# Kernel optimization log

Measured on AMD Instinct MI355X. Metric: run time of the kernel, lower is better.

The kernel has to match this reference:

```python
import jax, jax.numpy as jnp
import numpy as np

EPS_RMS = 1e-6
EPS_L2 = 1e-12  # torch F.normalize default eps


def _l2_normalize(x):
    n = jnp.sqrt(jnp.sum(x * x, axis=-1, keepdims=True))
    return x / jnp.maximum(n, EPS_L2)


def _dwconv(x, w, b):
    # depthwise Conv1d: x [B,L,D], w [D,1,K], b [D]; padding=K//2 (same length for odd K)
    K = w.shape[-1]
    y = jax.lax.conv_general_dilated(
        jnp.swapaxes(x, 1, 2), w, window_strides=(1,),
        padding=[(K // 2, K // 2)], feature_group_count=w.shape[0],
        dimension_numbers=('NCH', 'OIH', 'NCH'))
    return jnp.swapaxes(y + b[None, :, None], 1, 2)


def setup_inputs() -> dict:
    key = jax.random.key(0)
    ks = jax.random.split(key, 12)
    B, L, D, K = 8, 2048, 128, 3
    inp = {
        'x': jax.random.normal(ks[0], (B, L, D), dtype=jnp.float32),
        'state': jnp.zeros((B, D, D), dtype=jnp.float32),
        'W_in': jax.random.normal(ks[1], (4 * D, D), dtype=jnp.float32) * 0.02,
        'W_gate': jax.random.normal(ks[2], (2 * D, D), dtype=jnp.float32) * 0.02,
        'W_out': jax.random.normal(ks[3], (D, D), dtype=jnp.float32) * 0.02,
        'W_res': jax.random.normal(ks[4], (D, D), dtype=jnp.float32) * 0.02,
        'qconv_w': jax.random.normal(ks[5], (D, 1, K), dtype=jnp.float32) * 0.5,
        'qconv_b': jnp.zeros((D,), dtype=jnp.float32),
        'kconv_w': jax.random.normal(ks[6], (D, 1, K), dtype=jnp.float32) * 0.5,
        'kconv_b': jnp.zeros((D,), dtype=jnp.float32),
        'rms_w': jnp.ones((D,), dtype=jnp.float32),
    }
    return inp


def reference(x, state, W_in, W_gate, W_out, W_res,
              qconv_w, qconv_b, kconv_w, kconv_b, rms_w):
    B, L, D = x.shape
    residual = x @ W_res.T
    qkv = x @ W_in.T  # [B,L,4D]
    q, k, v, gate = jnp.split(qkv, 4, axis=-1)
    q = _l2_normalize(jax.nn.sigmoid(_dwconv(q, qconv_w, qconv_b)))
    k = _l2_normalize(jax.nn.sigmoid(_dwconv(k, kconv_w, kconv_b)))
    g = jax.nn.sigmoid(gate @ W_gate.T)  # [B,L,2D]
    alpha, beta = jnp.split(g, 2, axis=-1)

    # Delta-rule recurrence over time. State S [B,D,D] indexed S[b, v_dim, k_dim]:
    # S <- alpha_j * (S_ij - (S k)_i * beta_j k_j) + beta_j * v_i k_j ; out = silu(q @ S)
    def step(S, inp):
        q_t, k_t, v_t, a_t, b_t = inp  # each [B,D]
        Sk = jnp.einsum('bij,bj->bi', S, k_t)          # S @ k
        bk = b_t * k_t                                  # beta*k, column scaling
        S = a_t[:, None, :] * (S - Sk[:, :, None] * bk[:, None, :]) \
            + v_t[:, :, None] * bk[:, None, :]
        out_t = jax.nn.silu(jnp.einsum('bi,bij->bj', q_t, S))
        return S, out_t

    xs = tuple(jnp.swapaxes(a, 0, 1) for a in (q, k, v, alpha, beta))  # [L,B,D]
    S_fin, outs = jax.lax.scan(step, state, xs)
    out = jnp.swapaxes(outs, 0, 1) @ W_out.T  # [B,L,D]
    # dropout (p=0.125) is identity in eval mode
    out = out * jax.lax.rsqrt(jnp.mean(out * out, axis=-1, keepdims=True) + EPS_RMS) * rms_w
    out = out + residual
    return out, S_fin
```

## Files before the change

kernel.cpp:

```cpp
#include <hip/hip_runtime.h>
#include <hip/hip_bf16.h>
#include <math.h>

#define BB 8
#define LL 2048
#define LQ 512
#define DD 128

template <int CTRL>
__device__ __forceinline__ float dpp_add(float x) {
    int xi = __float_as_int(x);
    int yi = __builtin_amdgcn_update_dpp(xi, xi, CTRL, 0xF, 0xF, false);
    return x + __int_as_float(yi);
}
__device__ __forceinline__ float allreduce16(float p) {
    p = dpp_add<0xB1>(p);
    p = dpp_add<0x4E>(p);
    p = dpp_add<0x141>(p);
    p = dpp_add<0x140>(p);
    return p;
}
__device__ __forceinline__ float rlane(float p, int l) {
    return __int_as_float(__builtin_amdgcn_readlane(__float_as_int(p), l));
}

__global__ __launch_bounds__(256) void gemm_kernel(
    const float* __restrict__ X, long ldx, long sB, long sQ,
    const float* __restrict__ W,
    float* __restrict__ C, int ldc,
    int applySig)
{
    __shared__ float Xs[32 * 132];
    __shared__ float Ws[64 * 132];
    const int tid = threadIdx.x;
    const int m0 = blockIdx.x * 32;
    const int o0 = blockIdx.y * 64;
    {
        int row = tid >> 3, cg = tid & 7;
        int m = m0 + row;
        int b = m >> 11, t = m & 2047, qq = t >> 9, tl = t & 511;
        const float* src = X + (size_t)b * sB + (size_t)qq * sQ
                             + (size_t)tl * ldx + cg * 16;
        float* dst = Xs + row * 132 + cg * 16;
#pragma unroll
        for (int u = 0; u < 4; ++u)
            *(float4*)(dst + 4 * u) = *(const float4*)(src + 4 * u);
    }
    {
        int o = tid >> 2, cg = tid & 3;
        const float* src = W + (size_t)(o0 + o) * 128 + cg * 32;
        float* dst = Ws + o * 132 + cg * 32;
#pragma unroll
        for (int u = 0; u < 8; ++u)
            *(float4*)(dst + 4 * u) = *(const float4*)(src + 4 * u);
    }
    __syncthreads();
    const int tx = tid & 31, ty = tid >> 5;
    float acc[4][2] = {};
    const float* xb = Xs + (ty * 4) * 132;
    const float* wb = Ws + (tx * 2) * 132;
    for (int k0 = 0; k0 < 128; k0 += 4) {
        float4 xr[4], wr[2];
#pragma unroll
        for (int r = 0; r < 4; ++r) xr[r] = *(const float4*)(xb + r * 132 + k0);
#pragma unroll
        for (int cc = 0; cc < 2; ++cc) wr[cc] = *(const float4*)(wb + cc * 132 + k0);
#pragma unroll
        for (int r = 0; r < 4; ++r)
#pragma unroll
            for (int cc = 0; cc < 2; ++cc) {
                acc[r][cc] += xr[r].x * wr[cc].x + xr[r].y * wr[cc].y
                            + xr[r].z * wr[cc].z + xr[r].w * wr[cc].w;
            }
    }
#pragma unroll
    for (int r = 0; r < 4; ++r)
#pragma unroll
        for (int cc = 0; cc < 2; ++cc) {
            float v = acc[r][cc];
            if (applySig) v = 1.0f / (1.0f + __expf(-v));
            C[(size_t)(m0 + ty * 4 + r) * ldc + o0 + tx * 2 + cc] = v;
        }
}

__global__ __launch_bounds__(256) void convnorm_kernel(
    const float* __restrict__ qkv,
    const float* __restrict__ qw, const float* __restrict__ qb,
    const float* __restrict__ kw, const float* __restrict__ kb,
    const float* __restrict__ ab,
    float* __restrict__ pack)
{
    const int tid = threadIdx.x;
    const int lane = tid & 63;
    const int wid = tid >> 6;
    const int m = blockIdx.x * 4 + wid;
    const int l = m & (LL - 1);
    const int b = m >> 11;
    const int d0 = lane * 2;
    float yq0 = qb[d0], yq1 = qb[d0 + 1];
    float yk0 = kb[d0], yk1 = kb[d0 + 1];
#pragma unroll
    for (int tau = 0; tau < 3; ++tau) {
        int lp = l + tau - 1;
        if (lp >= 0 && lp < LL) {
            const float* base = qkv + (size_t)(m + tau - 1) * 512;
            yq0 += base[d0]       * qw[d0 * 3 + tau];
            yq1 += base[d0 + 1]   * qw[(d0 + 1) * 3 + tau];
            yk0 += base[128 + d0]     * kw[d0 * 3 + tau];
            yk1 += base[128 + d0 + 1] * kw[(d0 + 1) * 3 + tau];
        }
    }
    yq0 = 1.0f / (1.0f + __expf(-yq0));
    yq1 = 1.0f / (1.0f + __expf(-yq1));
    yk0 = 1.0f / (1.0f + __expf(-yk0));
    yk1 = 1.0f / (1.0f + __expf(-yk1));
    float sq = yq0 * yq0 + yq1 * yq1;
    float sk = yk0 * yk0 + yk1 * yk1;
#pragma unroll
    for (int msk = 1; msk <= 32; msk <<= 1) {
        sq += __shfl_xor(sq, msk);
        sk += __shfl_xor(sk, msk);
    }
    float rq = 1.0f / fmaxf(sqrtf(sq), 1e-12f);
    float rk = 1.0f / fmaxf(sqrtf(sk), 1e-12f);
    float k0n = yk0 * rk, k1n = yk1 * rk;
    float a0 = ab[(size_t)m * 256 + d0];
    float a1 = ab[(size_t)m * 256 + d0 + 1];
    float b0 = ab[(size_t)m * 256 + 128 + d0];
    float b1 = ab[(size_t)m * 256 + 128 + d0 + 1];
    float v0 = qkv[(size_t)m * 512 + 256 + d0];
    float v1 = qkv[(size_t)m * 512 + 256 + d0 + 1];
    float* P = pack + ((size_t)b * 512 + (l >> 2)) * 2560 + (l & 3);
    P[d0 * 4]              = k0n;      P[(d0 + 1) * 4]        = k1n;
    P[512 + d0 * 4]        = b0 * k0n; P[512 + (d0 + 1) * 4]  = b1 * k1n;
    P[1024 + d0 * 4]       = a0;       P[1024 + (d0 + 1) * 4] = a1;
    P[1536 + d0 * 4]       = yq0 * rq; P[1536 + (d0 + 1) * 4] = yq1 * rq;
    P[2048 + d0 * 4]       = v0;       P[2048 + (d0 + 1) * 4] = v1;
}

__global__ __launch_bounds__(64, 1) void recur1_kernel(
    const float* __restrict__ pack, const float* __restrict__ sin,
    __hip_bfloat16* __restrict__ pout, float* __restrict__ sout, int blk0)
{
    const int lane = threadIdx.x;
    const int b = blockIdx.x >> 7;
    const int g = blockIdx.x & 127;
    const int j0 = lane * 2;

    float SA[2];
    {
        const float* sp = sin + ((size_t)b * DD + g) * DD + j0;
        float2 t2 = *(const float2*)sp;
        SA[0] = t2.x; SA[1] = t2.y;
    }

    const float* P = pack + ((size_t)b * 512 + blk0) * 2560;
    __hip_bfloat16* po = pout + ((size_t)g * (BB * LQ) + (size_t)b * LQ) * DD + j0;

    float4 ka4[2][2], ma4[2][2], aa4[2][2];
    float4 qv4[2], vv4[2];

#define PREB(BF)                                                             \
    do {                                                                     \
        ka4[BF][0] = *(const float4*)(P + j0 * 4);                           \
        ka4[BF][1] = *(const float4*)(P + j0 * 4 + 4);                       \
        ma4[BF][0] = *(const float4*)(P + 512 + j0 * 4);                     \
        ma4[BF][1] = *(const float4*)(P + 512 + j0 * 4 + 4);                 \
        aa4[BF][0] = *(const float4*)(P + 1024 + j0 * 4);                    \
        aa4[BF][1] = *(const float4*)(P + 1024 + j0 * 4 + 4);                \
        qv4[BF]    = *(const float4*)(P + 1536 + g * 4);                     \
        vv4[BF]    = *(const float4*)(P + 2048 + g * 4);                     \
        P += 2560;                                                           \
        __builtin_amdgcn_sched_barrier(0);         \
    } while (0)

#define STEPQ(BF, CMP)                                                       \
    do {                                                                     \
        float e = SA[0] * ka4[BF][0].CMP;                                    \
        e = fmaf(SA[1], ka4[BF][1].CMP, e);                                  \
        float p = allreduce16(e);                                            \
        float sk = (rlane(p, 0) + rlane(p, 16))                              \
                 + (rlane(p, 32) + rlane(p, 48));                            \
        float vg = vv4[BF].CMP, qg = qv4[BF].CMP;                            \
        float a0 = aa4[BF][0].CMP, a1 = aa4[BF][1].CMP;                      \
        float w0 = fmaf(-a0, sk, vg);                                        \
        SA[0] = fmaf(ma4[BF][0].CMP, w0, a0 * SA[0]);                        \
        float w1 = fmaf(-a1, sk, vg);                                        \
        SA[1] = fmaf(ma4[BF][1].CMP, w1, a1 * SA[1]);                        \
        __hip_bfloat162 h2;                                                  \
        h2.x = __float2bfloat16(qg * SA[0]);                                 \
        h2.y = __float2bfloat16(qg * SA[1]);                                 \
        *(__hip_bfloat162*)po = h2;                                          \
        po += DD;                                                            \
    } while (0)

#define STEP4(BF) \
    do { STEPQ(BF, x); STEPQ(BF, y); STEPQ(BF, z); STEPQ(BF, w); } while (0)

    PREB(0);
    PREB(1);
    for (int tb = 0; tb < LQ / 4; tb += 2) {
        STEP4(0);
        PREB(0);
        STEP4(1);
        PREB(1);
    }
#undef PREB
#undef STEPQ
#undef STEP4

    {
        float* sp = sout + ((size_t)b * DD + g) * DD + j0;
        float2 o2 = {SA[0], SA[1]};
        *(float2*)sp = o2;
    }
}

__global__ __launch_bounds__(256) void combine_silu_kernel(
    const ushort* __restrict__ pout, float* __restrict__ ocbase, int q)
{
    const size_t NQ = (size_t)BB * LQ * DD;
    size_t idx = ((size_t)blockIdx.x * 256 + threadIdx.x) * 4;
    float s0 = 0, s1 = 0, s2 = 0, s3 = 0;
#pragma unroll 8
    for (int gi = 0; gi < 128; ++gi) {
        uint2 u = *(const uint2*)(pout + gi * NQ + idx);
        s0 += __uint_as_float((u.x & 0xffffu) << 16);
        s1 += __uint_as_float(u.x & 0xffff0000u);
        s2 += __uint_as_float((u.y & 0xffffu) << 16);
        s3 += __uint_as_float(u.y & 0xffff0000u);
    }
    float4 r;
    r.x = s0 / (1.0f + __expf(-s0));
    r.y = s1 / (1.0f + __expf(-s1));
    r.z = s2 / (1.0f + __expf(-s2));
    r.w = s3 / (1.0f + __expf(-s3));
    size_t b = idx >> 16;
    size_t rem = idx & ((size_t)LQ * DD - 1);
    float* dst = ocbase + b * (512ull * 2560) + (size_t)q * (128ull * 2560) + rem;
    *(float4*)dst = r;
}

__global__ __launch_bounds__(256) void rms_res_kernel(
    const float* __restrict__ y, const float* __restrict__ res,
    const float* __restrict__ rmsw, float* __restrict__ out)
{
    const int tid = threadIdx.x;
    const int lane = tid & 63;
    const int wid = tid >> 6;
    const int m = blockIdx.x * 4 + wid;
    const int d0 = lane * 2;
    size_t o = (size_t)m * DD + d0;
    float2 yv = *(const float2*)(y + o);
    float ss = yv.x * yv.x + yv.y * yv.y;
#pragma unroll
    for (int msk = 1; msk <= 32; msk <<= 1) ss += __shfl_xor(ss, msk);
    float r = rsqrtf(ss * (1.0f / 128.0f) + 1e-6f);
    float2 rv = *(const float2*)(res + o);
    out[o]     = yv.x * r * rmsw[d0]     + rv.x;
    out[o + 1] = yv.y * r * rmsw[d0 + 1] + rv.y;
}

extern "C" void kernel_launch(void* const* d_in, const int* in_sizes, int n_in,
                              void* d_out, int out_size, void* d_ws, size_t ws_size,
                              hipStream_t stream)
{
    const float* x      = (const float*)d_in[0];
    const float* state  = (const float*)d_in[1];
    const float* W_in   = (const float*)d_in[2];
    const float* W_gate = (const float*)d_in[3];
    const float* W_out  = (const float*)d_in[4];
    const float* W_res  = (const float*)d_in[5];
    const float* qcw    = (const float*)d_in[6];
    const float* qcb    = (const float*)d_in[7];
    const float* kcw    = (const float*)d_in[8];
    const float* kcb    = (const float*)d_in[9];
    const float* rmsw   = (const float*)d_in[10];
    float* out  = (float*)d_out;
    float* sfin = out + (size_t)BB * LL * DD;

    const size_t M = (size_t)BB * LL;
    char* base = (char*)d_ws;
    const size_t PACK_BYTES = M * 640 * 4;
    float* pack = (float*)base;
    char*  poreg = base + PACK_BYTES;
    float* qkv = (float*)poreg;
    float* abv = (float*)(poreg + M * 512 * 4);
    __hip_bfloat16* po = (__hip_bfloat16*)poreg;
    float* res = (float*)poreg;
    float* yb  = (float*)(poreg + M * DD * 4);

    dim3 blk(256);
    gemm_kernel<<<dim3(M / 32, 8), blk, 0, stream>>>(
        x, 128, 2048L * 128, 512L * 128, W_in, qkv, 512, 0);
    gemm_kernel<<<dim3(M / 32, 4), blk, 0, stream>>>(
        qkv + 384, 512, 2048L * 512, 512L * 512, W_gate, abv, 256, 1);
    convnorm_kernel<<<dim3(M / 4), blk, 0, stream>>>(qkv, qcw, qcb, kcw, kcb, abv, pack);
    for (int q = 0; q < 4; ++q) {
        const float* sin = (q == 0) ? state : sfin;
        recur1_kernel<<<dim3(BB * 128), dim3(64), 0, stream>>>(
            pack, sin, po, sfin, q * 128);
        combine_silu_kernel<<<dim3(512), blk, 0, stream>>>(
            (const ushort*)po, pack, q);
    }
    gemm_kernel<<<dim3(M / 32, 2), blk, 0, stream>>>(
        x, 128, 2048L * 128, 512L * 128, W_res, res, 128, 0);
    gemm_kernel<<<dim3(M / 32, 2), blk, 0, stream>>>(
        pack, 128, 512L * 2560, 128L * 2560, W_out, yb, 128, 0);
    rms_res_kernel<<<dim3(M / 4), blk, 0, stream>>>(yb, res, rmsw, out);
}
```

Measured before the change: 562.5 us.

## Batch four delta-rule steps per reduction using precomputed intra-block Gram terms

A new blockprep kernel precomputes, for each group of four timesteps, the pairwise k·(decayed beta*k) Gram coefficients and rescales k by the cumulative alpha products. The recurrence kernel then computes all four S·k dot products from the same state at once and resolves the intra-block dependencies with a small triangular solve. This takes the cross-lane reduction off the serial per-step critical path, issuing four independent reductions per block, and replaces readlane with swizzle/shuffle. It adds an extra kernel, some extra loads per block, and scratch space placed in the output buffer, which is overwritten later.

```diff
diff --git a/kernel.cpp b/kernel.cpp
--- a/kernel.cpp
+++ b/kernel.cpp
@@ -20,8 +20,10 @@
     p = dpp_add<0x140>(p);
     return p;
 }
-__device__ __forceinline__ float rlane(float p, int l) {
-    return __int_as_float(__builtin_amdgcn_readlane(__float_as_int(p), l));
+__device__ __forceinline__ float red_tail(float p) {
+    p += __int_as_float(__builtin_amdgcn_ds_swizzle(__float_as_int(p), 0x401F));
+    p += __shfl_xor(p, 32);
+    return p;
 }
 
 __global__ __launch_bounds__(256) void gemm_kernel(
@@ -138,8 +140,66 @@
     P[2048 + d0 * 4]       = v0;       P[2048 + (d0 + 1) * 4] = v1;
 }
 
+__global__ __launch_bounds__(256) void blockprep_kernel(
+    float* __restrict__ pack, float* __restrict__ gh)
+{
+    const int lane = threadIdx.x & 63;
+    const int w = threadIdx.x >> 6;
+    const int tbid = blockIdx.x * 4 + w;
+    const int j0 = lane * 2;
+    float* P = pack + (size_t)tbid * 2560;
+    float4 kc[2], mc[2], ac[2];
+    kc[0] = *(const float4*)(P + j0 * 4);
+    kc[1] = *(const float4*)(P + j0 * 4 + 4);
+    mc[0] = *(const float4*)(P + 512 + j0 * 4);
+    mc[1] = *(const float4*)(P + 512 + j0 * 4 + 4);
+    ac[0] = *(const float4*)(P + 1024 + j0 * 4);
+    ac[1] = *(const float4*)(P + 1024 + j0 * 4 + 4);
+    float s[12];
+#pragma unroll
+    for (int i = 0; i < 12; ++i) s[i] = 0.f;
+#pragma unroll
+    for (int c = 0; c < 2; ++c) {
+        const float k1 = kc[c].y, k2 = kc[c].z, k3 = kc[c].w;
+        const float m0 = mc[c].x, m1 = mc[c].y, m2 = mc[c].z;
+        const float a0 = ac[c].x, a1 = ac[c].y, a2 = ac[c].z;
+        float t  = m0, ta = a0 * m0;
+        s[0]  += t * k1;   s[1]  += ta * k1;
+        t *= a1; ta *= a1;
+        s[2]  += t * k2;   s[3]  += ta * k2;
+        t *= a2; ta *= a2;
+        s[4]  += t * k3;   s[5]  += ta * k3;
+        float u = m1, ua = a1 * m1;
+        s[6]  += u * k2;   s[7]  += ua * k2;
+        u *= a2; ua *= a2;
+        s[8]  += u * k3;   s[9]  += ua * k3;
+        s[10] += m2 * k3;  s[11] += a2 * m2 * k3;
+        const float p01 = a0, p012 = a0 * a1;
+        kc[c].y = k1 * p01;
+        kc[c].z = k2 * p012;
+        kc[c].w = k3 * (p012 * a2);
+    }
+#pragma unroll
+    for (int i = 0; i < 12; ++i)
+#pragma unroll
+        for (int msk = 1; msk <= 32; msk <<= 1)
+            s[i] += __shfl_xor(s[i], msk);
+    *(float4*)(P + j0 * 4)     = kc[0];
+    *(float4*)(P + j0 * 4 + 4) = kc[1];
+    if (lane == 0) {
+        float* q = gh + (size_t)tbid * 16;
+        float4 g0 = { s[0], s[1], s[2],  s[3]  };
+        float4 g1 = { s[4], s[5], s[6],  s[7]  };
+        float4 g2 = { s[8], s[9], s[10], s[11] };
+        *(float4*)(q)     = g0;
+        *(float4*)(q + 4) = g1;
+        *(float4*)(q + 8) = g2;
+    }
+}
+
 __global__ __launch_bounds__(64, 1) void recur1_kernel(
-    const float* __restrict__ pack, const float* __restrict__ sin,
+    const float* __restrict__ pack, const float* __restrict__ ghg,
+    const float* __restrict__ sin,
     __hip_bfloat16* __restrict__ pout, float* __restrict__ sout, int blk0)
 {
     const int lane = threadIdx.x;
@@ -154,39 +214,38 @@
         SA[0] = t2.x; SA[1] = t2.y;
     }
 
-    const float* P = pack + ((size_t)b * 512 + blk0) * 2560;
+    const float* P  = pack + ((size_t)b * 512 + blk0) * 2560;
+    const float* GH = ghg  + ((size_t)b * 512 + blk0) * 16;
     __hip_bfloat16* po = pout + ((size_t)g * (BB * LQ) + (size_t)b * LQ) * DD + j0;
 
-    float4 ka4[2][2], ma4[2][2], aa4[2][2];
-    float4 qv4[2], vv4[2];
+    float4 ka[2][2], ma[2][2], aa[2][2], qv[2], vv[2], gA[2], gB[2], gC[2];
 
 #define PREB(BF)                                                             \
     do {                                                                     \
-        ka4[BF][0] = *(const float4*)(P + j0 * 4);                           \
-        ka4[BF][1] = *(const float4*)(P + j0 * 4 + 4);                       \
-        ma4[BF][0] = *(const float4*)(P + 512 + j0 * 4);                     \
-        ma4[BF][1] = *(const float4*)(P + 512 + j0 * 4 + 4);                 \
-        aa4[BF][0] = *(const float4*)(P + 1024 + j0 * 4);                    \
-        aa4[BF][1] = *(const float4*)(P + 1024 + j0 * 4 + 4);                \
-        qv4[BF]    = *(const float4*)(P + 1536 + g * 4);                     \
-        vv4[BF]    = *(const float4*)(P + 2048 + g * 4);                     \
-        P += 2560;                                                           \
+        ka[BF][0] = *(const float4*)(P + j0 * 4);                            \
+        ka[BF][1] = *(const float4*)(P + j0 * 4 + 4);                        \
+        ma[BF][0] = *(const float4*)(P + 512 + j0 * 4);                      \
+        ma[BF][1] = *(const float4*)(P + 512 + j0 * 4 + 4);                  \
+        aa[BF][0] = *(const float4*)(P + 1024 + j0 * 4);                     \
+        aa[BF][1] = *(const float4*)(P + 1024 + j0 * 4 + 4);                 \
+        qv[BF]    = *(const float4*)(P + 1536 + g * 4);                      \
+        vv[BF]    = *(const float4*)(P + 2048 + g * 4);                      \
+        gA[BF]    = *(const float4*)(GH);                                    \
+        gB[BF]    = *(const float4*)(GH + 4);                                \
+        gC[BF]    = *(const float4*)(GH + 8);                                \
+        P += 2560; GH += 16;                                                 \
         __builtin_amdgcn_sched_barrier(0);         \
     } while (0)
 
-#define STEPQ(BF, CMP)                                                       \
+#define UPD(BF, CMP, SK)                                                     \
     do {                                                                     \
-        float e = SA[0] * ka4[BF][0].CMP;                                    \
-        e = fmaf(SA[1], ka4[BF][1].CMP, e);                                  \
-        float p = allreduce16(e);                                            \
-        float sk = (rlane(p, 0) + rlane(p, 16))                              \
-                 + (rlane(p, 32) + rlane(p, 48));                            \
-        float vg = vv4[BF].CMP, qg = qv4[BF].CMP;                            \
-        float a0 = aa4[BF][0].CMP, a1 = aa4[BF][1].CMP;                      \
-        float w0 = fmaf(-a0, sk, vg);                                        \
-        SA[0] = fmaf(ma4[BF][0].CMP, w0, a0 * SA[0]);                        \
-        float w1 = fmaf(-a1, sk, vg);                                        \
-        SA[1] = fmaf(ma4[BF][1].CMP, w1, a1 * SA[1]);                        \
+        const float a0 = aa[BF][0].CMP, a1 = aa[BF][1].CMP;                  \
+        const float m0 = ma[BF][0].CMP, m1 = ma[BF][1].CMP;                  \
+        const float vg = vv[BF].CMP, qg = qv[BF].CMP;                        \
+        float w0 = fmaf(-a0, SK, vg);                                        \
+        SA[0] = fmaf(m0, w0, a0 * SA[0]);                                    \
+        float w1 = fmaf(-a1, SK, vg);                                        \
+        SA[1] = fmaf(m1, w1, a1 * SA[1]);                                    \
         __hip_bfloat162 h2;                                                  \
         h2.x = __float2bfloat16(qg * SA[0]);                                 \
         h2.y = __float2bfloat16(qg * SA[1]);                                 \
@@ -194,20 +253,39 @@
         po += DD;                                                            \
     } while (0)
 
-#define STEP4(BF) \
-    do { STEPQ(BF, x); STEPQ(BF, y); STEPQ(BF, z); STEPQ(BF, w); } while (0)
+#define BLOCK(BF)                                                            \
+    do {                                                                     \
+        float E0 = fmaf(SA[1], ka[BF][1].x, SA[0] * ka[BF][0].x);            \
+        float E1 = fmaf(SA[1], ka[BF][1].y, SA[0] * ka[BF][0].y);            \
+        float E2 = fmaf(SA[1], ka[BF][1].z, SA[0] * ka[BF][0].z);            \
+        float E3 = fmaf(SA[1], ka[BF][1].w, SA[0] * ka[BF][0].w);            \
+        E0 = allreduce16(E0); E1 = allreduce16(E1);                          \
+        E2 = allreduce16(E2); E3 = allreduce16(E3);                          \
+        E0 = red_tail(E0); E1 = red_tail(E1);                                \
+        E2 = red_tail(E2); E3 = red_tail(E3);                                \
+        const float vg0 = vv[BF].x, vg1 = vv[BF].y, vg2 = vv[BF].z;          \
+        float u1 = vg0 * gA[BF].x;                                           \
+        float u2 = fmaf(vg1, gB[BF].z, vg0 * gA[BF].z);                      \
+        float u3 = fmaf(vg2, gC[BF].z, fmaf(vg1, gC[BF].x, vg0 * gB[BF].x)); \
+        float sk0 = E0;                                                      \
+        float sk1 = fmaf(-sk0, gA[BF].y, E1 + u1);                           \
+        float sk2 = fmaf(-sk1, gB[BF].w, fmaf(-sk0, gA[BF].w, E2 + u2));     \
+        float sk3 = fmaf(-sk2, gC[BF].w,                                     \
+                    fmaf(-sk1, gC[BF].y, fmaf(-sk0, gB[BF].y, E3 + u3)));    \
+        UPD(BF, x, sk0); UPD(BF, y, sk1); UPD(BF, z, sk2); UPD(BF, w, sk3);  \
+    } while (0)
 
     PREB(0);
     PREB(1);
     for (int tb = 0; tb < LQ / 4; tb += 2) {
-        STEP4(0);
+        BLOCK(0);
         PREB(0);
-        STEP4(1);
+        BLOCK(1);
         PREB(1);
     }
 #undef PREB
-#undef STEPQ
-#undef STEP4
+#undef UPD
+#undef BLOCK
 
     {
         float* sp = sout + ((size_t)b * DD + g) * DD + j0;
@@ -278,6 +356,7 @@
     const float* rmsw   = (const float*)d_in[10];
     float* out  = (float*)d_out;
     float* sfin = out + (size_t)BB * LL * DD;
+    float* ghs  = out;
 
     const size_t M = (size_t)BB * LL;
     char* base = (char*)d_ws;
@@ -296,10 +375,11 @@
     gemm_kernel<<<dim3(M / 32, 4), blk, 0, stream>>>(
         qkv + 384, 512, 2048L * 512, 512L * 512, W_gate, abv, 256, 1);
     convnorm_kernel<<<dim3(M / 4), blk, 0, stream>>>(qkv, qcw, qcb, kcw, kcb, abv, pack);
+    blockprep_kernel<<<dim3(1024), blk, 0, stream>>>(pack, ghs);
     for (int q = 0; q < 4; ++q) {
         const float* sin = (q == 0) ? state : sfin;
         recur1_kernel<<<dim3(BB * 128), dim3(64), 0, stream>>>(
-            pack, sin, po, sfin, q * 128);
+            pack, ghs, sin, po, sfin, q * 128);
         combine_silu_kernel<<<dim3(512), blk, 0, stream>>>(
             (const ushort*)po, pack, q);
     }
```

New measurement: 577.9 us. 2.7% more time.
